# Kernel optimization log

Measured on AMD Instinct MI355X. Metric: run time of the kernel, lower is better.

The kernel has to match this reference:

```python
import jax, jax.numpy as jnp
import numpy as np

N_NODES = 10000
N_EDGES = 320000
D = 256
D_OUT = 256
NUM_REL = 2


def setup_inputs() -> dict:
    key = jax.random.key(0)
    ks = jax.random.split(key, 16)
    s = 1.0 / np.sqrt(D)
    inp = {}
    inp['feat'] = jax.random.normal(ks[0], (N_NODES, D), dtype=jnp.float32)
    inp['src'] = jax.random.randint(ks[1], (N_EDGES,), 0, N_NODES, dtype=jnp.int32)
    inp['dst'] = jax.random.randint(ks[2], (N_EDGES,), 0, N_NODES, dtype=jnp.int32)
    inp['rel'] = jax.random.randint(ks[3], (N_EDGES,), 0, NUM_REL, dtype=jnp.int32)
    # per-relation edgeNN: ONE tied Linear(D, D) applied twice with relu
    inp['W_rel'] = jax.random.normal(ks[4], (NUM_REL, D, D), dtype=jnp.float32) * s
    inp['b_rel'] = jax.random.normal(ks[5], (NUM_REL, D), dtype=jnp.float32) * s
    # LSTM (single step from zero state: W_hh contributes 0, omitted)
    inp['W_ih'] = jax.random.normal(ks[6], (4 * D, D), dtype=jnp.float32) * s
    inp['b_ih'] = jax.random.normal(ks[7], (4 * D,), dtype=jnp.float32) * s
    inp['b_hh'] = jax.random.normal(ks[8], (4 * D,), dtype=jnp.float32) * s
    # global_update MLP: D -> D/2 -> D/2 -> D_OUT
    h = D // 2
    inp['W1'] = jax.random.normal(ks[9], (h, D), dtype=jnp.float32) * s
    inp['b1'] = jax.random.normal(ks[10], (h,), dtype=jnp.float32) * s
    inp['W2'] = jax.random.normal(ks[11], (h, h), dtype=jnp.float32) * (1.0 / np.sqrt(h))
    inp['b2'] = jax.random.normal(ks[12], (h,), dtype=jnp.float32) * (1.0 / np.sqrt(h))
    inp['W3'] = jax.random.normal(ks[13], (D_OUT, h), dtype=jnp.float32) * (1.0 / np.sqrt(h))
    inp['b3'] = jax.random.normal(ks[14], (D_OUT,), dtype=jnp.float32) * (1.0 / np.sqrt(h))
    return inp


def reference(feat, src, dst, rel, W_rel, b_rel, W_ih, b_ih, b_hh,
              W1, b1, W2, b2, W3, b3):
    n_nodes = feat.shape[0]
    # ---- message: per-edge relation-typed tied-weight MLP ----
    S = feat[src]  # [E, D] gather of source features

    def edge_nn(x, W, b):
        h = jax.nn.relu(x @ W.T + b)
        return jax.nn.relu(h @ W.T + b)  # same lin1 applied twice (tied)

    msgs = jnp.zeros_like(S)
    for r in range(W_rel.shape[0]):  # small fixed relation count
        msgs = jnp.where((rel == r)[:, None], edge_nn(S, W_rel[r], b_rel[r]), msgs)

    # ---- reduce: scatter-sum into destination nodes ----
    agg = jax.ops.segment_sum(msgs, dst, num_segments=n_nodes)  # [N, D]

    # ---- apply: per-node single-step LSTM from zero (h0, c0) ----
    gates = agg @ W_ih.T + b_ih + b_hh  # [N, 4D], torch gate order i,f,g,o
    i, f, g, o = jnp.split(gates, 4, axis=-1)
    c = jax.nn.sigmoid(i) * jnp.tanh(g)  # f * c0 = 0
    hn = jax.nn.sigmoid(o) * jnp.tanh(c)  # [N, D]

    # ---- global_update MLP ----
    x = jax.nn.relu(hn @ W1.T + b1)
    x = jax.nn.relu(x @ W2.T + b2)
    return x @ W3.T + b3  # [N, D_OUT]
```

## Files before the change

### kernel.cpp

```cpp
#include <hip/hip_runtime.h>
#include <hip/hip_bf16.h>

#define N_NODES 10000
#define N_EDGES 320000
#define D 256

typedef __attribute__((ext_vector_type(8))) _Float16 f16x8;
typedef __attribute__((ext_vector_type(4))) _Float16 f16x4;
typedef __attribute__((ext_vector_type(4))) float f32x4;

__device__ __forceinline__ void async_copy16(const void* g, void* l) {
  __builtin_amdgcn_global_load_lds(
      (const __attribute__((address_space(1))) unsigned int*)g,
      (__attribute__((address_space(3))) unsigned int*)l, 16, 0, 0);
}

template<int ROWS, int WAVES>
__device__ __forceinline__ void stage_tile(const _Float16* __restrict__ Wb, int k0, int K,
                                           _Float16* Bs, int wave, int lane) {
  const int sr = lane >> 2, ss = lane & 3;
#pragma unroll
  for (int grp = wave; grp < ROWS / 16; grp += WAVES) {
    int r = grp * 16 + sr;
    int gq = ss ^ ((r >> 1) & 3);
    async_copy16(Wb + (size_t)r * K + k0 + gq * 8, Bs + grp * 512);
  }
}
__device__ __forceinline__ f16x8 read_B(const _Float16* Bs, int r, int quad) {
  return *(const f16x8*)(Bs + r * 32 + (quad ^ ((r >> 1) & 3)) * 8);
}

__device__ __forceinline__ float fast_sigmoid(float x) {
  return __builtin_amdgcn_rcpf(1.f + __expf(-x));
}
__device__ __forceinline__ float fast_tanh(float x) {
  float ax = fabsf(x);
  float e = __expf(-2.f * ax);
  float t = (1.f - e) * __builtin_amdgcn_rcpf(1.f + e);
  return copysignf(t, x);
}

__global__ __launch_bounds__(512) void prep_cast(
    int* __restrict__ cnt,
    const float* __restrict__ W_rel, const float* __restrict__ W_ih,
    const float* __restrict__ b_ih, const float* __restrict__ b_hh,
    const float* __restrict__ W1, const float* __restrict__ W2,
    const float* __restrict__ W3,
    _Float16* __restrict__ W_relh, _Float16* __restrict__ Wg,
    float* __restrict__ bg,
    _Float16* __restrict__ W1h, _Float16* __restrict__ W2h,
    _Float16* __restrict__ W3h) {
  int i = blockIdx.x * 512 + threadIdx.x;
  if (i < 10240) { if (i < N_NODES) cnt[i] = 0; return; }
  i -= 10240;
  if (i < 131072) { W_relh[i] = (_Float16)W_rel[i]; return; }
  i -= 131072;
  if (i < 196608) {
    int p = i >> 8, k = i & 255;
    int t = p / 48, rem = p - t * 48;
    int phase = rem >> 4, u = rem & 15;
    int orig = t * 16 + u + (phase == 1 ? 512 : (phase == 2 ? 768 : 0));
    Wg[i] = (_Float16)W_ih[orig * 256 + k]; return;
  }
  i -= 196608;
  if (i < 32768) { W1h[i] = (_Float16)W1[i]; return; }
  i -= 32768;
  if (i < 16384) { W2h[i] = (_Float16)W2[i]; return; }
  i -= 16384;
  if (i < 32768) { W3h[i] = (_Float16)W3[i]; return; }
  i -= 32768;
  if (i < 768) {
    int t = i / 48, rem = i - t * 48;
    int phase = rem >> 4, u = rem & 15;
    int orig = t * 16 + u + (phase == 1 ? 512 : (phase == 2 ? 768 : 0));
    bg[i] = b_ih[orig] + b_hh[orig];
  }
}

#define NB_GEMM 626
__global__ __launch_bounds__(256, 4) void edge_fill(
    const float* __restrict__ feat, const _Float16* __restrict__ W_relh,
    const float* __restrict__ b_rel, _Float16* __restrict__ Mh,
    const int* __restrict__ dst, const int* __restrict__ src,
    const int* __restrict__ rel,
    int* __restrict__ cnt, unsigned int* __restrict__ rowoff)
{
  __shared__ _Float16 Hs[32 * 266];
  __shared__ alignas(16) _Float16 Bs[256 * 32];
  const int b = blockIdx.x;
  if (b >= NB_GEMM) {
    int i = (b - NB_GEMM) * 256 + threadIdx.x;
    int v = dst[i];
    int pos = atomicAdd(&cnt[v], 1);
    if (pos < 128)
      rowoff[(v << 7) + pos] = (unsigned int)((rel[i] * N_NODES + src[i]) * D);
    return;
  }
  const int t = threadIdx.x;
  const int wave = t >> 6, lane = t & 63;
  const int quad = lane >> 4, lrow = lane & 15;
  const int z = (b >= 313) ? 1 : 0;
  const int m0 = (b - z * 313) * 32;
  const _Float16* Wb = W_relh + z * 65536;
  const float* bb = b_rel + z * 256;
  const int wn = wave * 64;

  int ar0 = m0 + lrow;      if (ar0 > N_NODES - 1) ar0 = N_NODES - 1;
  int ar1 = m0 + 16 + lrow; if (ar1 > N_NODES - 1) ar1 = N_NODES - 1;
  const float* fr0 = feat + (size_t)ar0 * 256;
  const float* fr1 = feat + (size_t)ar1 * 256;

  f32x4 acc[2][4];
#pragma unroll
  for (int i = 0; i < 2; ++i)
#pragma unroll
    for (int j = 0; j < 4; ++j) acc[i][j] = (f32x4)0.0f;

#pragma unroll
  for (int kc = 0; kc < 8; ++kc) {
    stage_tile<256, 4>(Wb, kc * 32, 256, Bs, wave, lane);
    float4 u0 = *(const float4*)(fr0 + kc * 32 + quad * 8);
    float4 u1 = *(const float4*)(fr0 + kc * 32 + quad * 8 + 4);
    float4 v0 = *(const float4*)(fr1 + kc * 32 + quad * 8);
    float4 v1 = *(const float4*)(fr1 + kc * 32 + quad * 8 + 4);
    f16x8 af0, af1;
    af0[0] = (_Float16)u0.x; af0[1] = (_Float16)u0.y; af0[2] = (_Float16)u0.z; af0[3] = (_Float16)u0.w;
    af0[4] = (_Float16)u1.x; af0[5] = (_Float16)u1.y; af0[6] = (_Float16)u1.z; af0[7] = (_Float16)u1.w;
    af1[0] = (_Float16)v0.x; af1[1] = (_Float16)v0.y; af1[2] = (_Float16)v0.z; af1[3] = (_Float16)v0.w;
    af1[4] = (_Float16)v1.x; af1[5] = (_Float16)v1.y; af1[6] = (_Float16)v1.z; af1[7] = (_Float16)v1.w;
    __syncthreads();
#pragma unroll
    for (int j = 0; j < 4; ++j) {
      f16x8 bf = read_B(Bs, wn + j * 16 + lrow, quad);
      acc[0][j] = __builtin_amdgcn_mfma_f32_16x16x32_f16(af0, bf, acc[0][j], 0, 0, 0);
      acc[1][j] = __builtin_amdgcn_mfma_f32_16x16x32_f16(af1, bf, acc[1][j], 0, 0, 0);
    }
    __syncthreads();
  }
#pragma unroll
  for (int i = 0; i < 2; ++i) {
    int rb = i * 16 + quad * 4;
#pragma unroll
    for (int j = 0; j < 4; ++j) {
      int col = wn + j * 16 + lrow;
      float bv = bb[col];
#pragma unroll
      for (int reg = 0; reg < 4; ++reg) {
        Hs[(rb + reg) * 266 + col] = (_Float16)fmaxf(acc[i][j][reg] + bv, 0.f);
        acc[i][j][reg] = 0.f;
      }
    }
  }
  __syncthreads();

#pragma unroll
  for (int kc = 0; kc < 8; ++kc) {
    stage_tile<256, 4>(Wb, kc * 32, 256, Bs, wave, lane);
    f16x8 af0 = *(const f16x8*)(Hs + lrow * 266 + kc * 32 + quad * 8);
    f16x8 af1 = *(const f16x8*)(Hs + (16 + lrow) * 266 + kc * 32 + quad * 8);
    __syncthreads();
#pragma unroll
    for (int j = 0; j < 4; ++j) {
      f16x8 bf = read_B(Bs, wn + j * 16 + lrow, quad);
      acc[0][j] = __builtin_amdgcn_mfma_f32_16x16x32_f16(af0, bf, acc[0][j], 0, 0, 0);
      acc[1][j] = __builtin_amdgcn_mfma_f32_16x16x32_f16(af1, bf, acc[1][j], 0, 0, 0);
    }
    __syncthreads();
  }
  _Float16* Mo = Mh + (size_t)z * (N_NODES * D);
#pragma unroll
  for (int i = 0; i < 2; ++i) {
    int rb = m0 + i * 16 + quad * 4;
#pragma unroll
    for (int j = 0; j < 4; ++j) {
      int col = wn + j * 16 + lrow;
      float bv = bb[col];
#pragma unroll
      for (int reg = 0; reg < 4; ++reg) {
        int gm = rb + reg;
        if (gm < N_NODES)
          Mo[(size_t)gm * D + col] = (_Float16)fmaxf(acc[i][j][reg] + bv, 0.f);
      }
    }
  }
}

__global__ __launch_bounds__(256) void agg_kernel(const int* __restrict__ cnt,
                                                  const unsigned int* __restrict__ rowoff,
                                                  const _Float16* __restrict__ Mh,
                                                  _Float16* __restrict__ aggh) {
  __shared__ float part[4][256];
  const int node = blockIdx.x;
  const int wave = threadIdx.x >> 6, lane = threadIdx.x & 63;
  const int base = node << 7;
  const int deg = cnt[node];
  float a0 = 0.f, a1 = 0.f, a2 = 0.f, a3 = 0.f;
  for (int j = wave; j < deg; j += 4) {
    unsigned int off = rowoff[base + j];
    f16x4 v = *(const f16x4*)(Mh + (size_t)off + lane * 4);
    a0 += (float)v[0]; a1 += (float)v[1]; a2 += (float)v[2]; a3 += (float)v[3];
  }
  *(float4*)&part[wave][lane * 4] = make_float4(a0, a1, a2, a3);
  __syncthreads();
  if (wave == 0) {
    float4 p0 = *(const float4*)&part[0][lane * 4];
    float4 p1 = *(const float4*)&part[1][lane * 4];
    float4 p2 = *(const float4*)&part[2][lane * 4];
    float4 p3 = *(const float4*)&part[3][lane * 4];
    f16x4 o;
    o[0] = (_Float16)(p0.x + p1.x + p2.x + p3.x);
    o[1] = (_Float16)(p0.y + p1.y + p2.y + p3.y);
    o[2] = (_Float16)(p0.z + p1.z + p2.z + p3.z);
    o[3] = (_Float16)(p0.w + p1.w + p2.w + p3.w);
    *(f16x4*)(aggh + (size_t)node * D + lane * 4) = o;
  }
}

__global__ __launch_bounds__(256) void tail(
    const _Float16* __restrict__ aggh,
    const _Float16* __restrict__ Wg, const float* __restrict__ bg,
    const _Float16* __restrict__ W1h, const float* __restrict__ b1,
    const _Float16* __restrict__ W2h, const float* __restrict__ b2,
    const _Float16* __restrict__ W3h, const float* __restrict__ b3,
    float* __restrict__ out)
{
  __shared__ alignas(16) _Float16 Ws[768 * 32];
  __shared__ _Float16 Hn[16 * 266];
  __shared__ _Float16 Xs[16 * 138];
  __shared__ _Float16 X2s[16 * 138];
  const int t = threadIdx.x;
  const int wave = t >> 6, lane = t & 63;
  const int quad = lane >> 4, lrow = lane & 15;
  const int r0 = blockIdx.x * 16;

  {
    f16x8 af[8];
#pragma unroll
    for (int kc = 0; kc < 8; ++kc)
      af[kc] = *(const f16x8*)(aggh + (size_t)(r0 + lrow) * 256 + kc * 32 + quad * 8);
    f32x4 acc[12];
#pragma unroll
    for (int j = 0; j < 12; ++j) acc[j] = (f32x4)0.0f;
#pragma unroll
    for (int kc = 0; kc < 8; ++kc) {
      stage_tile<768, 4>(Wg, kc * 32, 256, Ws, wave, lane);
      __syncthreads();
#pragma unroll
      for (int j = 0; j < 12; ++j) {
        f16x8 bf = read_B(Ws, (wave * 12 + j) * 16 + lrow, quad);
        acc[j] = __builtin_amdgcn_mfma_f32_16x16x32_f16(af[kc], bf, acc[j], 0, 0, 0);
      }
      __syncthreads();
    }
#pragma unroll
    for (int p = 0; p < 4; ++p) {
      float bvi = bg[(wave * 12 + 3 * p + 0) * 16 + lrow];
      float bvg = bg[(wave * 12 + 3 * p + 1) * 16 + lrow];
      float bvo = bg[(wave * 12 + 3 * p + 2) * 16 + lrow];
      int dcol = (wave * 4 + p) * 16 + lrow;
#pragma unroll
      for (int reg = 0; reg < 4; ++reg) {
        float vi = acc[3 * p + 0][reg] + bvi;
        float vg = acc[3 * p + 1][reg] + bvg;
        float vo = acc[3 * p + 2][reg] + bvo;
        float c = fast_sigmoid(vi) * fast_tanh(vg);
        Hn[(quad * 4 + reg) * 266 + dcol] = (_Float16)(fast_sigmoid(vo) * fast_tanh(c));
      }
    }
  }
  __syncthreads();

  {
    f16x8 af[8];
#pragma unroll
    for (int kc = 0; kc < 8; ++kc)
      af[kc] = *(const f16x8*)(Hn + lrow * 266 + kc * 32 + quad * 8);
    f32x4 acc[2];
    acc[0] = (f32x4)0.0f; acc[1] = (f32x4)0.0f;
#pragma unroll
    for (int kc = 0; kc < 8; ++kc) {
      stage_tile<128, 4>(W1h, kc * 32, 256, Ws, wave, lane);
      __syncthreads();
#pragma unroll
      for (int j = 0; j < 2; ++j) {
        f16x8 bf = read_B(Ws, wave * 32 + j * 16 + lrow, quad);
        acc[j] = __builtin_amdgcn_mfma_f32_16x16x32_f16(af[kc], bf, acc[j], 0, 0, 0);
      }
      __syncthreads();
    }
#pragma unroll
    for (int j = 0; j < 2; ++j) {
      int col = wave * 32 + j * 16 + lrow;
      float bv = b1[col];
#pragma unroll
      for (int reg = 0; reg < 4; ++reg)
        Xs[(quad * 4 + reg) * 138 + col] = (_Float16)fmaxf(acc[j][reg] + bv, 0.f);
    }
  }
  __syncthreads();

  {
    f16x8 af[4];
#pragma unroll
    for (int kc = 0; kc < 4; ++kc)
      af[kc] = *(const f16x8*)(Xs + lrow * 138 + kc * 32 + quad * 8);
    f32x4 acc[2];
    acc[0] = (f32x4)0.0f; acc[1] = (f32x4)0.0f;
#pragma unroll
    for (int kc = 0; kc < 4; ++kc) {
      stage_tile<128, 4>(W2h, kc * 32, 128, Ws, wave, lane);
      __syncthreads();
#pragma unroll
      for (int j = 0; j < 2; ++j) {
        f16x8 bf = read_B(Ws, wave * 32 + j * 16 + lrow, quad);
        acc[j] = __builtin_amdgcn_mfma_f32_16x16x32_f16(af[kc], bf, acc[j], 0, 0, 0);
      }
      __syncthreads();
    }
#pragma unroll
    for (int j = 0; j < 2; ++j) {
      int col = wave * 32 + j * 16 + lrow;
      float bv = b2[col];
#pragma unroll
      for (int reg = 0; reg < 4; ++reg)
        X2s[(quad * 4 + reg) * 138 + col] = (_Float16)fmaxf(acc[j][reg] + bv, 0.f);
    }
  }
  __syncthreads();

  {
    f16x8 af[4];
#pragma unroll
    for (int kc = 0; kc < 4; ++kc)
      af[kc] = *(const f16x8*)(X2s + lrow * 138 + kc * 32 + quad * 8);
    f32x4 acc[4];
#pragma unroll
    for (int j = 0; j < 4; ++j) acc[j] = (f32x4)0.0f;
#pragma unroll
    for (int kc = 0; kc < 4; ++kc) {
      stage_tile<256, 4>(W3h, kc * 32, 128, Ws, wave, lane);
      __syncthreads();
#pragma unroll
      for (int j = 0; j < 4; ++j) {
        f16x8 bf = read_B(Ws, wave * 64 + j * 16 + lrow, quad);
        acc[j] = __builtin_amdgcn_mfma_f32_16x16x32_f16(af[kc], bf, acc[j], 0, 0, 0);
      }
      __syncthreads();
    }
#pragma unroll
    for (int j = 0; j < 4; ++j) {
      int col = wave * 64 + j * 16 + lrow;
      float bv = b3[col];
#pragma unroll
      for (int reg = 0; reg < 4; ++reg)
        out[(size_t)(r0 + quad * 4 + reg) * 256 + col] = acc[j][reg] + bv;
    }
  }
}

extern "C" void kernel_launch(void* const* d_in, const int* in_sizes, int n_in,
                              void* d_out, int out_size, void* d_ws, size_t ws_size,
                              hipStream_t stream) {
  const float* feat  = (const float*)d_in[0];
  const int* src = (const int*)d_in[1];
  const int* dst = (const int*)d_in[2];
  const int* rel = (const int*)d_in[3];
  const float* W_rel = (const float*)d_in[4];
  const float* b_rel = (const float*)d_in[5];
  const float* W_ih  = (const float*)d_in[6];
  const float* b_ih  = (const float*)d_in[7];
  const float* b_hh  = (const float*)d_in[8];
  const float* W1 = (const float*)d_in[9];
  const float* b1 = (const float*)d_in[10];
  const float* W2 = (const float*)d_in[11];
  const float* b2 = (const float*)d_in[12];
  const float* W3 = (const float*)d_in[13];
  const float* b3 = (const float*)d_in[14];
  float* out = (float*)d_out;

  char* ws = (char*)d_ws;
  _Float16* Mh   = (_Float16*)(ws);
  _Float16* aggh = (_Float16*)(ws + 10240000);
  char* wsb = ws + 15360000;
  _Float16* W_relh = (_Float16*)(wsb);
  _Float16* Wg     = (_Float16*)(wsb + 262144);
  _Float16* W1h    = (_Float16*)(wsb + 655360);
  _Float16* W2h    = (_Float16*)(wsb + 720896);
  _Float16* W3h    = (_Float16*)(wsb + 753664);
  float*    bg     = (float*)(wsb + 819200);
  int*      cnt    = (int*)(wsb + 822272);
  unsigned int* rowoff = (unsigned int*)(wsb + 862272);

  prep_cast<<<822, 512, 0, stream>>>(cnt, W_rel, W_ih, b_ih, b_hh, W1, W2, W3,
                                     W_relh, Wg, bg, W1h, W2h, W3h);
  edge_fill<<<1876, 256, 0, stream>>>(feat, W_relh, b_rel, Mh,
                                      dst, src, rel, cnt, rowoff);
  agg_kernel<<<N_NODES, 256, 0, stream>>>(cnt, rowoff, Mh, aggh);
  tail<<<625, 256, 0, stream>>>(aggh, Wg, bg, W1h, b1, W2h, b2, W3h, b3, out);
}
```

Baseline: 198.6 us.

## Make edge_fill persistent with full relation weight resident in LDS

Relaunches edge_fill as 256 persistent blocks of 512 threads. Each block stages the entire 256x256 fp16 relation weight into LDS once and reuses it for up to three 32-row node tiles and both tied layers, instead of re-staging a 32-column slab per k-chunk with barriers. The edge bucketing (atomic counting and rowoff writes) is folded into each block's prologue rather than running in separate blocks. This removes repeated weight staging and most syncs, at the cost of about 145KB of LDS per block, lower occupancy, and fewer blocks than CUs.

Result: slower. 204.6 us (+3.1%).

```diff
diff --git a/kernel.cpp b/kernel.cpp
--- a/kernel.cpp
+++ b/kernel.cpp
@@ -77,111 +77,101 @@
   }
 }
 
-#define NB_GEMM 626
-__global__ __launch_bounds__(256, 4) void edge_fill(
+__global__ __launch_bounds__(512, 2) void edge_fill(
     const float* __restrict__ feat, const _Float16* __restrict__ W_relh,
     const float* __restrict__ b_rel, _Float16* __restrict__ Mh,
     const int* __restrict__ dst, const int* __restrict__ src,
     const int* __restrict__ rel,
     int* __restrict__ cnt, unsigned int* __restrict__ rowoff)
 {
+  __shared__ alignas(16) _Float16 Ws[8 * 8192];
   __shared__ _Float16 Hs[32 * 266];
-  __shared__ alignas(16) _Float16 Bs[256 * 32];
   const int b = blockIdx.x;
-  if (b >= NB_GEMM) {
-    int i = (b - NB_GEMM) * 256 + threadIdx.x;
-    int v = dst[i];
-    int pos = atomicAdd(&cnt[v], 1);
-    if (pos < 128)
-      rowoff[(v << 7) + pos] = (unsigned int)((rel[i] * N_NODES + src[i]) * D);
-    return;
-  }
   const int t = threadIdx.x;
   const int wave = t >> 6, lane = t & 63;
   const int quad = lane >> 4, lrow = lane & 15;
-  const int z = (b >= 313) ? 1 : 0;
-  const int m0 = (b - z * 313) * 32;
+  const int z = (b >= 128) ? 1 : 0;
+  const int bl = b - z * 128;
   const _Float16* Wb = W_relh + z * 65536;
   const float* bb = b_rel + z * 256;
-  const int wn = wave * 64;
-
-  int ar0 = m0 + lrow;      if (ar0 > N_NODES - 1) ar0 = N_NODES - 1;
-  int ar1 = m0 + 16 + lrow; if (ar1 > N_NODES - 1) ar1 = N_NODES - 1;
-  const float* fr0 = feat + (size_t)ar0 * 256;
-  const float* fr1 = feat + (size_t)ar1 * 256;
-
-  f32x4 acc[2][4];
-#pragma unroll
-  for (int i = 0; i < 2; ++i)
-#pragma unroll
-    for (int j = 0; j < 4; ++j) acc[i][j] = (f32x4)0.0f;
-
-#pragma unroll
-  for (int kc = 0; kc < 8; ++kc) {
-    stage_tile<256, 4>(Wb, kc * 32, 256, Bs, wave, lane);
-    float4 u0 = *(const float4*)(fr0 + kc * 32 + quad * 8);
-    float4 u1 = *(const float4*)(fr0 + kc * 32 + quad * 8 + 4);
-    float4 v0 = *(const float4*)(fr1 + kc * 32 + quad * 8);
-    float4 v1 = *(const float4*)(fr1 + kc * 32 + quad * 8 + 4);
-    f16x8 af0, af1;
-    af0[0] = (_Float16)u0.x; af0[1] = (_Float16)u0.y; af0[2] = (_Float16)u0.z; af0[3] = (_Float16)u0.w;
-    af0[4] = (_Float16)u1.x; af0[5] = (_Float16)u1.y; af0[6] = (_Float16)u1.z; af0[7] = (_Float16)u1.w;
-    af1[0] = (_Float16)v0.x; af1[1] = (_Float16)v0.y; af1[2] = (_Float16)v0.z; af1[3] = (_Float16)v0.w;
-    af1[4] = (_Float16)v1.x; af1[5] = (_Float16)v1.y; af1[6] = (_Float16)v1.z; af1[7] = (_Float16)v1.w;
-    __syncthreads();
-#pragma unroll
-    for (int j = 0; j < 4; ++j) {
-      f16x8 bf = read_B(Bs, wn + j * 16 + lrow, quad);
-      acc[0][j] = __builtin_amdgcn_mfma_f32_16x16x32_f16(af0, bf, acc[0][j], 0, 0, 0);
-      acc[1][j] = __builtin_amdgcn_mfma_f32_16x16x32_f16(af1, bf, acc[1][j], 0, 0, 0);
-    }
-    __syncthreads();
-  }
-#pragma unroll
-  for (int i = 0; i < 2; ++i) {
-    int rb = i * 16 + quad * 4;
+
+#pragma unroll
+  for (int kc = 0; kc < 8; ++kc)
+    stage_tile<256, 8>(Wb, kc * 32, 256, Ws + kc * 8192, wave, lane);
+
+  {
+    const int ebase = b * 1250;
+    for (int e = t; e < 1250; e += 512) {
+      int idx = ebase + e;
+      int v = dst[idx];
+      int pos = atomicAdd(&cnt[v], 1);
+      if (pos < 128)
+        rowoff[(v << 7) + pos] = (unsigned int)((rel[idx] * N_NODES + src[idx]) * D);
+    }
+  }
+  __syncthreads();
+
+  const int wm = (wave >> 2) * 16;
+  const int wn = (wave & 3) * 64;
+  _Float16* Mo = Mh + (size_t)z * (N_NODES * D);
+
+  for (int t3 = 0; t3 < 3; ++t3) {
+    int tile = t3 * 128 + bl;
+    if (tile >= 313) break;
+    const int m0 = tile * 32;
+    int ar = m0 + wm + lrow; if (ar > N_NODES - 1) ar = N_NODES - 1;
+    const float* fr = feat + (size_t)ar * 256;
+
+    f32x4 acc[4];
+#pragma unroll
+    for (int j = 0; j < 4; ++j) acc[j] = (f32x4)0.0f;
+
+#pragma unroll
+    for (int kc = 0; kc < 8; ++kc) {
+      float4 u0 = *(const float4*)(fr + kc * 32 + quad * 8);
+      float4 u1 = *(const float4*)(fr + kc * 32 + quad * 8 + 4);
+      f16x8 af;
+      af[0] = (_Float16)u0.x; af[1] = (_Float16)u0.y; af[2] = (_Float16)u0.z; af[3] = (_Float16)u0.w;
+      af[4] = (_Float16)u1.x; af[5] = (_Float16)u1.y; af[6] = (_Float16)u1.z; af[7] = (_Float16)u1.w;
+#pragma unroll
+      for (int j = 0; j < 4; ++j) {
+        f16x8 bf = read_B(Ws + kc * 8192, wn + j * 16 + lrow, quad);
+        acc[j] = __builtin_amdgcn_mfma_f32_16x16x32_f16(af, bf, acc[j], 0, 0, 0);
+      }
+    }
 #pragma unroll
     for (int j = 0; j < 4; ++j) {
       int col = wn + j * 16 + lrow;
       float bv = bb[col];
 #pragma unroll
       for (int reg = 0; reg < 4; ++reg) {
-        Hs[(rb + reg) * 266 + col] = (_Float16)fmaxf(acc[i][j][reg] + bv, 0.f);
-        acc[i][j][reg] = 0.f;
-      }
-    }
-  }
-  __syncthreads();
-
-#pragma unroll
-  for (int kc = 0; kc < 8; ++kc) {
-    stage_tile<256, 4>(Wb, kc * 32, 256, Bs, wave, lane);
-    f16x8 af0 = *(const f16x8*)(Hs + lrow * 266 + kc * 32 + quad * 8);
-    f16x8 af1 = *(const f16x8*)(Hs + (16 + lrow) * 266 + kc * 32 + quad * 8);
+        Hs[(wm + quad * 4 + reg) * 266 + col] = (_Float16)fmaxf(acc[j][reg] + bv, 0.f);
+        acc[j][reg] = 0.f;
+      }
+    }
     __syncthreads();
-#pragma unroll
-    for (int j = 0; j < 4; ++j) {
-      f16x8 bf = read_B(Bs, wn + j * 16 + lrow, quad);
-      acc[0][j] = __builtin_amdgcn_mfma_f32_16x16x32_f16(af0, bf, acc[0][j], 0, 0, 0);
-      acc[1][j] = __builtin_amdgcn_mfma_f32_16x16x32_f16(af1, bf, acc[1][j], 0, 0, 0);
-    }
-    __syncthreads();
-  }
-  _Float16* Mo = Mh + (size_t)z * (N_NODES * D);
-#pragma unroll
-  for (int i = 0; i < 2; ++i) {
-    int rb = m0 + i * 16 + quad * 4;
+
+#pragma unroll
+    for (int kc = 0; kc < 8; ++kc) {
+      f16x8 af = *(const f16x8*)(Hs + (wm + lrow) * 266 + kc * 32 + quad * 8);
+#pragma unroll
+      for (int j = 0; j < 4; ++j) {
+        f16x8 bf = read_B(Ws + kc * 8192, wn + j * 16 + lrow, quad);
+        acc[j] = __builtin_amdgcn_mfma_f32_16x16x32_f16(af, bf, acc[j], 0, 0, 0);
+      }
+    }
 #pragma unroll
     for (int j = 0; j < 4; ++j) {
       int col = wn + j * 16 + lrow;
       float bv = bb[col];
 #pragma unroll
       for (int reg = 0; reg < 4; ++reg) {
-        int gm = rb + reg;
+        int gm = m0 + wm + quad * 4 + reg;
         if (gm < N_NODES)
-          Mo[(size_t)gm * D + col] = (_Float16)fmaxf(acc[i][j][reg] + bv, 0.f);
-      }
-    }
+          Mo[(size_t)gm * D + col] = (_Float16)fmaxf(acc[j][reg] + bv, 0.f);
+      }
+    }
+    __syncthreads();
   }
 }
 
@@ -393,8 +383,8 @@
 
   prep_cast<<<822, 512, 0, stream>>>(cnt, W_rel, W_ih, b_ih, b_hh, W1, W2, W3,
                                      W_relh, Wg, bg, W1h, W2h, W3h);
-  edge_fill<<<1876, 256, 0, stream>>>(feat, W_relh, b_rel, Mh,
-                                      dst, src, rel, cnt, rowoff);
+  edge_fill<<<256, 512, 0, stream>>>(feat, W_relh, b_rel, Mh,
+                                     dst, src, rel, cnt, rowoff);
   agg_kernel<<<N_NODES, 256, 0, stream>>>(cnt, rowoff, Mh, aggh);
   tail<<<625, 256, 0, stream>>>(aggh, Wg, bg, W1h, b1, W2h, b2, W3h, b3, out);
 }
```

## Load GEMM weight fragments directly from global memory instead of LDS staging

Applied to the files above, without the earlier changes.

Removes the LDS staging of weight tiles (async global-to-LDS copies with swizzle) in both the edge GEMM and tail kernels. Each wave now reads its B fragments straight from global memory, relying on L2/L1 caching of the small fp16 weight matrices. This drops the per-k-chunk __syncthreads pairs and frees LDS, which may raise occupancy. The cost is redundant global loads of the same weights across blocks, and exposed load latency with no software pipelining. The edge kernel's occupancy hint in launch_bounds is also dropped.

New measurement: 221.5 us. +11.5%, slower.

```diff
diff --git a/kernel.cpp b/kernel.cpp
--- a/kernel.cpp
+++ b/kernel.cpp
@@ -9,25 +9,9 @@
 typedef __attribute__((ext_vector_type(4))) _Float16 f16x4;
 typedef __attribute__((ext_vector_type(4))) float f32x4;
 
-__device__ __forceinline__ void async_copy16(const void* g, void* l) {
-  __builtin_amdgcn_global_load_lds(
-      (const __attribute__((address_space(1))) unsigned int*)g,
-      (__attribute__((address_space(3))) unsigned int*)l, 16, 0, 0);
-}
-
-template<int ROWS, int WAVES>
-__device__ __forceinline__ void stage_tile(const _Float16* __restrict__ Wb, int k0, int K,
-                                           _Float16* Bs, int wave, int lane) {
-  const int sr = lane >> 2, ss = lane & 3;
-#pragma unroll
-  for (int grp = wave; grp < ROWS / 16; grp += WAVES) {
-    int r = grp * 16 + sr;
-    int gq = ss ^ ((r >> 1) & 3);
-    async_copy16(Wb + (size_t)r * K + k0 + gq * 8, Bs + grp * 512);
-  }
-}
-__device__ __forceinline__ f16x8 read_B(const _Float16* Bs, int r, int quad) {
-  return *(const f16x8*)(Bs + r * 32 + (quad ^ ((r >> 1) & 3)) * 8);
+__device__ __forceinline__ f16x8 load_B(const _Float16* __restrict__ W, int row, int K,
+                                        int kc, int quad) {
+  return *(const f16x8*)(W + (size_t)row * K + kc * 32 + quad * 8);
 }
 
 __device__ __forceinline__ float fast_sigmoid(float x) {
@@ -78,7 +62,7 @@
 }
 
 #define NB_GEMM 626
-__global__ __launch_bounds__(256, 4) void edge_fill(
+__global__ __launch_bounds__(256) void edge_fill(
     const float* __restrict__ feat, const _Float16* __restrict__ W_relh,
     const float* __restrict__ b_rel, _Float16* __restrict__ Mh,
     const int* __restrict__ dst, const int* __restrict__ src,
@@ -86,7 +70,6 @@
     int* __restrict__ cnt, unsigned int* __restrict__ rowoff)
 {
   __shared__ _Float16 Hs[32 * 266];
-  __shared__ alignas(16) _Float16 Bs[256 * 32];
   const int b = blockIdx.x;
   if (b >= NB_GEMM) {
     int i = (b - NB_GEMM) * 256 + threadIdx.x;
@@ -118,7 +101,6 @@
 
 #pragma unroll
   for (int kc = 0; kc < 8; ++kc) {
-    stage_tile<256, 4>(Wb, kc * 32, 256, Bs, wave, lane);
     float4 u0 = *(const float4*)(fr0 + kc * 32 + quad * 8);
     float4 u1 = *(const float4*)(fr0 + kc * 32 + quad * 8 + 4);
     float4 v0 = *(const float4*)(fr1 + kc * 32 + quad * 8);
@@ -128,14 +110,12 @@
     af0[4] = (_Float16)u1.x; af0[5] = (_Float16)u1.y; af0[6] = (_Float16)u1.z; af0[7] = (_Float16)u1.w;
     af1[0] = (_Float16)v0.x; af1[1] = (_Float16)v0.y; af1[2] = (_Float16)v0.z; af1[3] = (_Float16)v0.w;
     af1[4] = (_Float16)v1.x; af1[5] = (_Float16)v1.y; af1[6] = (_Float16)v1.z; af1[7] = (_Float16)v1.w;
-    __syncthreads();
-#pragma unroll
-    for (int j = 0; j < 4; ++j) {
-      f16x8 bf = read_B(Bs, wn + j * 16 + lrow, quad);
+#pragma unroll
+    for (int j = 0; j < 4; ++j) {
+      f16x8 bf = load_B(Wb, wn + j * 16 + lrow, 256, kc, quad);
       acc[0][j] = __builtin_amdgcn_mfma_f32_16x16x32_f16(af0, bf, acc[0][j], 0, 0, 0);
       acc[1][j] = __builtin_amdgcn_mfma_f32_16x16x32_f16(af1, bf, acc[1][j], 0, 0, 0);
     }
-    __syncthreads();
   }
 #pragma unroll
   for (int i = 0; i < 2; ++i) {
@@ -155,17 +135,14 @@
 
 #pragma unroll
   for (int kc = 0; kc < 8; ++kc) {
-    stage_tile<256, 4>(Wb, kc * 32, 256, Bs, wave, lane);
     f16x8 af0 = *(const f16x8*)(Hs + lrow * 266 + kc * 32 + quad * 8);
     f16x8 af1 = *(const f16x8*)(Hs + (16 + lrow) * 266 + kc * 32 + quad * 8);
-    __syncthreads();
-#pragma unroll
-    for (int j = 0; j < 4; ++j) {
-      f16x8 bf = read_B(Bs, wn + j * 16 + lrow, quad);
+#pragma unroll
+    for (int j = 0; j < 4; ++j) {
+      f16x8 bf = load_B(Wb, wn + j * 16 + lrow, 256, kc, quad);
       acc[0][j] = __builtin_amdgcn_mfma_f32_16x16x32_f16(af0, bf, acc[0][j], 0, 0, 0);
       acc[1][j] = __builtin_amdgcn_mfma_f32_16x16x32_f16(af1, bf, acc[1][j], 0, 0, 0);
     }
-    __syncthreads();
   }
   _Float16* Mo = Mh + (size_t)z * (N_NODES * D);
 #pragma unroll
@@ -224,7 +201,6 @@
     const _Float16* __restrict__ W3h, const float* __restrict__ b3,
     float* __restrict__ out)
 {
-  __shared__ alignas(16) _Float16 Ws[768 * 32];
   __shared__ _Float16 Hn[16 * 266];
   __shared__ _Float16 Xs[16 * 138];
   __shared__ _Float16 X2s[16 * 138];
@@ -243,14 +219,11 @@
     for (int j = 0; j < 12; ++j) acc[j] = (f32x4)0.0f;
 #pragma unroll
     for (int kc = 0; kc < 8; ++kc) {
-      stage_tile<768, 4>(Wg, kc * 32, 256, Ws, wave, lane);
-      __syncthreads();
 #pragma unroll
       for (int j = 0; j < 12; ++j) {
-        f16x8 bf = read_B(Ws, (wave * 12 + j) * 16 + lrow, quad);
+        f16x8 bf = load_B(Wg, (wave * 12 + j) * 16 + lrow, 256, kc, quad);
         acc[j] = __builtin_amdgcn_mfma_f32_16x16x32_f16(af[kc], bf, acc[j], 0, 0, 0);
       }
-      __syncthreads();
     }
 #pragma unroll
     for (int p = 0; p < 4; ++p) {
@@ -279,14 +252,11 @@
     acc[0] = (f32x4)0.0f; acc[1] = (f32x4)0.0f;
 #pragma unroll
     for (int kc = 0; kc < 8; ++kc) {
-      stage_tile<128, 4>(W1h, kc * 32, 256, Ws, wave, lane);
-      __syncthreads();
 #pragma unroll
       for (int j = 0; j < 2; ++j) {
-        f16x8 bf = read_B(Ws, wave * 32 + j * 16 + lrow, quad);
+        f16x8 bf = load_B(W1h, wave * 32 + j * 16 + lrow, 256, kc, quad);
         acc[j] = __builtin_amdgcn_mfma_f32_16x16x32_f16(af[kc], bf, acc[j], 0, 0, 0);
       }
-      __syncthreads();
     }
 #pragma unroll
     for (int j = 0; j < 2; ++j) {
@@ -308,14 +278,11 @@
     acc[0] = (f32x4)0.0f; acc[1] = (f32x4)0.0f;
 #pragma unroll
     for (int kc = 0; kc < 4; ++kc) {
-      stage_tile<128, 4>(W2h, kc * 32, 128, Ws, wave, lane);
-      __syncthreads();
 #pragma unroll
       for (int j = 0; j < 2; ++j) {
-        f16x8 bf = read_B(Ws, wave * 32 + j * 16 + lrow, quad);
+        f16x8 bf = load_B(W2h, wave * 32 + j * 16 + lrow, 128, kc, quad);
         acc[j] = __builtin_amdgcn_mfma_f32_16x16x32_f16(af[kc], bf, acc[j], 0, 0, 0);
       }
-      __syncthreads();
     }
 #pragma unroll
     for (int j = 0; j < 2; ++j) {
@@ -338,14 +305,11 @@
     for (int j = 0; j < 4; ++j) acc[j] = (f32x4)0.0f;
 #pragma unroll
     for (int kc = 0; kc < 4; ++kc) {
-      stage_tile<256, 4>(W3h, kc * 32, 128, Ws, wave, lane);
-      __syncthreads();
 #pragma unroll
       for (int j = 0; j < 4; ++j) {
-        f16x8 bf = read_B(Ws, wave * 64 + j * 16 + lrow, quad);
+        f16x8 bf = load_B(W3h, wave * 64 + j * 16 + lrow, 128, kc, quad);
         acc[j] = __builtin_amdgcn_mfma_f32_16x16x32_f16(af[kc], bf, acc[j], 0, 0, 0);
       }
-      __syncthreads();
     }
 #pragma unroll
     for (int j = 0; j < 4; ++j) {
```
